# Optimization experiments

Measured on AMD Instinct MI355X. Metric: run time of the kernel, lower is better.

## Reference

```python
import jax, jax.numpy as jnp
import numpy as np

B, N_FED, INPUT_DIM, LATENT_DIM = 8192, 16384, 1024, 512


def setup_inputs() -> dict:
    key = jax.random.key(0)
    k1, k2, k3 = jax.random.split(key, 3)
    enc = jax.random.normal(k1, (B, LATENT_DIM), dtype=jnp.float32)
    X_fed = jax.random.normal(k2, (N_FED, INPUT_DIM), dtype=jnp.float32)
    # torch.rand -> uniform [0, 1)
    domain_diff = jax.random.uniform(k3, (INPUT_DIM, LATENT_DIM), dtype=jnp.float32)
    return {"enc": enc, "X_fed": X_fed, "domain_diff": domain_diff}


def reference(enc, X_fed, domain_diff):
    # K = V = X_fed @ domain_diff  (computed once; torch source computes it twice)
    kv = X_fed @ domain_diff                      # (N_fed, latent)
    scores = jnp.einsum('bd,nd->bn', enc, kv) / enc.shape[1]  # scale by latent_dim
    attn = jax.nn.softmax(scores, axis=1)         # softmax over N_fed axis
    z = attn @ kv                                 # (B, latent)
    return z
```

## Files before the change

kernel.cpp:

```cpp
#include <hip/hip_runtime.h>
#include <hip/hip_bf16.h>
#include <stdint.h>

#define ENC_B 8192
#define NFED  16384
#define INDIM 1024
#define LAT   512
#define SCALE (1.0f/512.0f)

typedef __attribute__((ext_vector_type(4))) float f32x4;
typedef __attribute__((ext_vector_type(8))) short short8;
typedef __attribute__((ext_vector_type(4))) short short4_t;

static __device__ __forceinline__ short f2bf(float x){
  union { float f; uint32_t u; } v; v.f = x;
  uint32_t r = v.u + 0x7FFFu + ((v.u >> 16) & 1u);
  return (short)(r >> 16);
}

static __device__ __forceinline__ void gload16(const void* g, void* l){
  __builtin_amdgcn_global_load_lds(
      (const __attribute__((address_space(1))) void*)g,
      (__attribute__((address_space(3))) void*)l, 16, 0, 0);
}

__global__ void ddT_kernel(const float* __restrict__ dd, short* __restrict__ ddT){
  const int n = blockIdx.x;
  for (int k = threadIdx.x; k < INDIM; k += 256)
    ddT[(size_t)n*INDIM + k] = f2bf(dd[(size_t)k*LAT + n]);
}

__global__ __launch_bounds__(256) void encb_kernel(const float* __restrict__ enc,
                                                   short* __restrict__ encb){
  const int gid = blockIdx.x*256 + threadIdx.x;
  const size_t base = (size_t)gid * 8;
  float4 v0 = *(const float4*)(enc + base);
  float4 v1 = *(const float4*)(enc + base + 4);
  short8 s;
  s[0]=f2bf(v0.x*SCALE); s[1]=f2bf(v0.y*SCALE); s[2]=f2bf(v0.z*SCALE); s[3]=f2bf(v0.w*SCALE);
  s[4]=f2bf(v1.x*SCALE); s[5]=f2bf(v1.y*SCALE); s[6]=f2bf(v1.z*SCALE); s[7]=f2bf(v1.w*SCALE);
  *(short8*)(encb + base) = s;
}

__global__ __launch_bounds__(256, 2) void kv_gemm_kernel(const float* __restrict__ X,
                                                         const short* __restrict__ ddT,
                                                         short* __restrict__ kv){
  __shared__ __align__(16) short As[128*40];
  __shared__ __align__(16) short Bs[128*40];
  const int t = threadIdx.x;
  const int lane = t & 63, w = t >> 6;
  const int lr = lane & 15, lg = lane >> 4;
  const int m0 = (blockIdx.x >> 2) * 128;
  const int n0 = (blockIdx.x & 3) * 128;
  const int wm = (w >> 1) * 64, wn = (w & 1) * 64;
  f32x4 acc[4][4];
  #pragma unroll
  for (int i=0;i<4;++i)
    #pragma unroll
    for (int j=0;j<4;++j) acc[i][j] = (f32x4){0.f,0.f,0.f,0.f};

  for (int k0 = 0; k0 < INDIM; k0 += 32) {
    #pragma unroll
    for (int i = 0; i < 4; ++i) {
      int idx = t + i*256;
      int row = idx >> 3, c4 = (idx & 7)*4;
      float4 v = *(const float4*)(X + (size_t)(m0+row)*INDIM + k0 + c4);
      short4_t s; s[0]=f2bf(v.x); s[1]=f2bf(v.y); s[2]=f2bf(v.z); s[3]=f2bf(v.w);
      *(short4_t*)(As + row*40 + c4) = s;
    }
    #pragma unroll
    for (int i = 0; i < 2; ++i) {
      int idx = t + i*256;
      int row = idx >> 2, c8 = (idx & 3)*8;
      *(uint4*)(Bs + row*40 + c8) = *(const uint4*)(ddT + (size_t)(n0+row)*INDIM + k0 + c8);
    }
    __syncthreads();
    short8 a[4], b[4];
    #pragma unroll
    for (int i=0;i<4;++i) a[i] = *(short8*)(As + (wm + i*16 + lr)*40 + lg*8);
    #pragma unroll
    for (int i=0;i<4;++i) b[i] = *(short8*)(Bs + (wn + i*16 + lr)*40 + lg*8);
    #pragma unroll
    for (int i=0;i<4;++i)
      #pragma unroll
      for (int j=0;j<4;++j)
        acc[i][j] = __builtin_amdgcn_mfma_f32_16x16x32_bf16(a[i], b[j], acc[i][j], 0,0,0);
    __syncthreads();
  }
  #pragma unroll
  for (int i=0;i<4;++i)
    #pragma unroll
    for (int j=0;j<4;++j)
      #pragma unroll
      for (int r=0;r<4;++r)
        kv[(size_t)(m0 + wm + i*16 + lg*4 + r)*LAT + n0 + wn + j*16 + lr] = f2bf(acc[i][j][r]);
}

__global__ __launch_bounds__(256) void kvT_kernel(const short* __restrict__ kv,
                                                  short* __restrict__ kvT){
  __shared__ short tile[64][72];
  const int t = threadIdx.x;
  const int bn = blockIdx.x & (NFED/64 - 1);
  const int bd = blockIdx.x / (NFED/64);
  #pragma unroll
  for (int i=0;i<2;++i){
    int idx = t + i*256; int row = idx >> 3, cc = (idx & 7)*8;
    *(uint4*)&tile[row][cc] = *(const uint4*)(kv + (size_t)(bn*64+row)*LAT + bd*64 + cc);
  }
  __syncthreads();
  #pragma unroll
  for (int i=0;i<2;++i){
    int idx = t + i*256; int drow = idx >> 3, nn = (idx & 7)*8;
    short8 v;
    #pragma unroll
    for (int j=0;j<8;++j) v[j] = tile[nn+j][drow];
    *(short8*)(kvT + (size_t)(bd*64+drow)*NFED + bn*64 + nn) = v;
  }
}

__global__ __launch_bounds__(256, 4) void s_gemm_kernel(const short* __restrict__ encb,
                                                        const short* __restrict__ kv,
                                                        short* __restrict__ Pc,
                                                        float* __restrict__ lpart,
                                                        int cbase, int chunk){
  __shared__ __align__(16) short As[128*32];
  __shared__ __align__(16) short Bs[128*32];
  __shared__ float lsum[128][2];
  const int t = threadIdx.x;
  const int lane = t & 63, w = t >> 6;
  const int lr = lane & 15, lg = lane >> 4;
  const int m0 = blockIdx.y * 128;
  const int n0g = cbase + blockIdx.x * 128;
  const int wm = (w >> 1) * 64, wn = (w & 1) * 64;

  const int sr = lane >> 2, sc = (lane & 3) * 8;
  const char* Asrc0 = (const char*)(encb + (size_t)(m0 + w*16      + sr)*LAT + sc);
  const char* Asrc1 = (const char*)(encb + (size_t)(m0 + (4+w)*16  + sr)*LAT + sc);
  const char* Bsrc0 = (const char*)(kv   + (size_t)(n0g + w*16     + sr)*LAT + sc);
  const char* Bsrc1 = (const char*)(kv   + (size_t)(n0g + (4+w)*16 + sr)*LAT + sc);
  char* AsD0 = (char*)As + w*1024;  char* AsD1 = (char*)As + (4+w)*1024;
  char* BsD0 = (char*)Bs + w*1024;  char* BsD1 = (char*)Bs + (4+w)*1024;

  f32x4 acc[4][4];
  #pragma unroll
  for (int i=0;i<4;++i)
    #pragma unroll
    for (int j=0;j<4;++j) acc[i][j] = (f32x4){0.f,0.f,0.f,0.f};

  for (int k0 = 0; k0 < LAT; k0 += 32) {
    gload16(Asrc0, AsD0); gload16(Asrc1, AsD1);
    gload16(Bsrc0, BsD0); gload16(Bsrc1, BsD1);
    Asrc0 += 64; Asrc1 += 64; Bsrc0 += 64; Bsrc1 += 64;
    __syncthreads();
    short8 a[4], b[4];
    #pragma unroll
    for (int i=0;i<4;++i) a[i] = *(short8*)((char*)As + (wm + i*16 + lr)*64 + lg*16);
    #pragma unroll
    for (int i=0;i<4;++i) b[i] = *(short8*)((char*)Bs + (wn + i*16 + lr)*64 + lg*16);
    #pragma unroll
    for (int i=0;i<4;++i)
      #pragma unroll
      for (int j=0;j<4;++j)
        acc[i][j] = __builtin_amdgcn_mfma_f32_16x16x32_bf16(a[i], b[j], acc[i][j], 0,0,0);
    __syncthreads();
  }

  float psum[4][4];
  #pragma unroll
  for (int i=0;i<4;++i)
    #pragma unroll
    for (int r=0;r<4;++r) psum[i][r] = 0.f;

  const int collocal0 = blockIdx.x * 128 + wn;
  #pragma unroll
  for (int i=0;i<4;++i)
    #pragma unroll
    for (int j=0;j<4;++j)
      #pragma unroll
      for (int r=0;r<4;++r) {
        float p = __expf(acc[i][j][r]);
        psum[i][r] += p;
        Pc[(size_t)(m0 + wm + i*16 + lg*4 + r)*chunk + collocal0 + j*16 + lr] = f2bf(p);
      }
  #pragma unroll
  for (int i=0;i<4;++i)
    #pragma unroll
    for (int r=0;r<4;++r) {
      float v = psum[i][r];
      v += __shfl_xor(v, 1, 16); v += __shfl_xor(v, 2, 16);
      v += __shfl_xor(v, 4, 16); v += __shfl_xor(v, 8, 16);
      if (lr == 0) lsum[wm + i*16 + lg*4 + r][w & 1] = v;
    }
  __syncthreads();
  if (t < 128) {
    int jsl = (cbase >> 7) + blockIdx.x;
    lpart[(size_t)jsl*ENC_B + m0 + t] = lsum[t][0] + lsum[t][1];
  }
}

__global__ __launch_bounds__(256, 4) void z_gemm_kernel(const short* __restrict__ kvT,
                                                        const short* __restrict__ Pc,
                                                        float* __restrict__ zpart,
                                                        int cbase, int chunk, int first){
  __shared__ __align__(16) short As[128*32];
  __shared__ __align__(16) short Bs[128*32];
  const int t = threadIdx.x;
  const int lane = t & 63, w = t >> 6;
  const int lr = lane & 15, lg = lane >> 4;
  const int n0 = blockIdx.x * 128;
  const int m0 = blockIdx.y * 128;
  const int s  = blockIdx.z;
  const int klocal0 = s * (chunk >> 2);
  const int wm = (w >> 1) * 64, wn = (w & 1) * 64;

  const int sr = lane >> 2, sc = (lane & 3) * 8;
  const char* Asrc0 = (const char*)(kvT + (size_t)(m0 + w*16      + sr)*NFED + cbase + klocal0 + sc);
  const char* Asrc1 = (const char*)(kvT + (size_t)(m0 + (4+w)*16  + sr)*NFED + cbase + klocal0 + sc);
  const char* Bsrc0 = (const char*)(Pc  + (size_t)(n0 + w*16      + sr)*chunk + klocal0 + sc);
  const char* Bsrc1 = (const char*)(Pc  + (size_t)(n0 + (4+w)*16  + sr)*chunk + klocal0 + sc);
  char* AsD0 = (char*)As + w*1024;  char* AsD1 = (char*)As + (4+w)*1024;
  char* BsD0 = (char*)Bs + w*1024;  char* BsD1 = (char*)Bs + (4+w)*1024;

  f32x4 acc[4][4];
  #pragma unroll
  for (int i=0;i<4;++i)
    #pragma unroll
    for (int j=0;j<4;++j) acc[i][j] = (f32x4){0.f,0.f,0.f,0.f};

  const int ksteps = chunk >> 7;
  for (int ks = 0; ks < ksteps; ++ks) {
    gload16(Asrc0, AsD0); gload16(Asrc1, AsD1);
    gload16(Bsrc0, BsD0); gload16(Bsrc1, BsD1);
    Asrc0 += 64; Asrc1 += 64; Bsrc0 += 64; Bsrc1 += 64;
    __syncthreads();
    short8 a[4], b[4];
    #pragma unroll
    for (int i=0;i<4;++i) a[i] = *(short8*)((char*)As + (wm + i*16 + lr)*64 + lg*16);
    #pragma unroll
    for (int i=0;i<4;++i) b[i] = *(short8*)((char*)Bs + (wn + i*16 + lr)*64 + lg*16);
    #pragma unroll
    for (int i=0;i<4;++i)
      #pragma unroll
      for (int j=0;j<4;++j)
        acc[i][j] = __builtin_amdgcn_mfma_f32_16x16x32_bf16(a[i], b[j], acc[i][j], 0,0,0);
    __syncthreads();
  }

  #pragma unroll
  for (int i=0;i<4;++i)
    #pragma unroll
    for (int j=0;j<4;++j)
      #pragma unroll
      for (int r=0;r<4;++r) {
        size_t idx = ((size_t)s*LAT + m0 + wm + i*16 + lg*4 + r)*ENC_B
                   + n0 + wn + j*16 + lr;
        if (first) zpart[idx] = acc[i][j][r];
        else       zpart[idx] += acc[i][j][r];
      }
}

__global__ __launch_bounds__(256) void lred_kernel(const float* __restrict__ lpart,
                                                   float* __restrict__ linv){
  const int row = blockIdx.x*256 + threadIdx.x;
  float sum = 0.f;
  for (int j = 0; j < NFED/128; ++j)
    sum += lpart[(size_t)j*ENC_B + row];
  linv[row] = 1.0f / sum;
}

__global__ __launch_bounds__(256) void zcomb_kernel(const float* __restrict__ zpart,
                                                    const float* __restrict__ linv,
                                                    float* __restrict__ out){
  __shared__ float tile[64][65];
  const int t = threadIdx.x;
  const int bx = blockIdx.x;
  const int by = blockIdx.y;
  const size_t sstr = (size_t)LAT*ENC_B;
  #pragma unroll
  for (int i=0;i<4;++i){
    int idx = t + i*256;
    int dr = idx >> 4, rc = (idx & 15)*4;
    const float* p0 = zpart + (size_t)(by*64+dr)*ENC_B + bx*64 + rc;
    float4 a = *(const float4*)p0;
    float4 b = *(const float4*)(p0 + sstr);
    float4 c = *(const float4*)(p0 + 2*sstr);
    float4 d = *(const float4*)(p0 + 3*sstr);
    tile[dr][rc+0] = (a.x+b.x)+(c.x+d.x); tile[dr][rc+1] = (a.y+b.y)+(c.y+d.y);
    tile[dr][rc+2] = (a.z+b.z)+(c.z+d.z); tile[dr][rc+3] = (a.w+b.w)+(c.w+d.w);
  }
  __syncthreads();
  #pragma unroll
  for (int i=0;i<4;++i){
    int idx = t + i*256;
    int rr = idx >> 4, dc = (idx & 15)*4;
    float li = linv[bx*64 + rr];
    float4 o;
    o.x = tile[dc+0][rr]*li; o.y = tile[dc+1][rr]*li;
    o.z = tile[dc+2][rr]*li; o.w = tile[dc+3][rr]*li;
    *(float4*)(out + (size_t)(bx*64+rr)*LAT + by*64 + dc) = o;
  }
}

extern "C" void kernel_launch(void* const* d_in, const int* in_sizes, int n_in,
                              void* d_out, int out_size, void* d_ws, size_t ws_size,
                              hipStream_t stream) {
  const float* enc = (const float*)d_in[0];
  const float* X   = (const float*)d_in[1];
  const float* dd  = (const float*)d_in[2];
  float* out = (float*)d_out;

  short* kvb   = (short*)d_ws;
  short* kvT   = (short*)((char*)d_ws + 16777216);
  short* encb  = (short*)((char*)d_ws + 33554432);
  float* lpart = (float*)((char*)d_ws + 41943040);
  short* ddT   = (short*)((char*)d_ws + 41943040);
  float* linv  = (float*)((char*)d_ws + 46137344);
  float* zpart = (float*)((char*)d_ws + 50331648);
  short* Pc    = (short*)((char*)d_ws + 117440512);

  int chunk;
  if      (ws_size >= (size_t)117440512 + (size_t)4096*ENC_B*2) chunk = 4096;
  else if (ws_size >= (size_t)117440512 + (size_t)2048*ENC_B*2) chunk = 2048;
  else                                                          chunk = 1024;

  ddT_kernel<<<LAT, 256, 0, stream>>>(dd, ddT);
  kv_gemm_kernel<<<(NFED/128)*(LAT/128), 256, 0, stream>>>(X, ddT, kvb);
  kvT_kernel<<<(NFED/64)*(LAT/64), 256, 0, stream>>>(kvb, kvT);
  encb_kernel<<<ENC_B*LAT/(256*8), 256, 0, stream>>>(enc, encb);

  const int nc = NFED / chunk;
  for (int c = 0; c < nc; ++c) {
    s_gemm_kernel<<<dim3(chunk/128, ENC_B/128), 256, 0, stream>>>(
        encb, kvb, Pc, lpart, c*chunk, chunk);
    z_gemm_kernel<<<dim3(ENC_B/128, LAT/128, 4), 256, 0, stream>>>(
        kvT, Pc, zpart, c*chunk, chunk, (c == 0) ? 1 : 0);
  }
  lred_kernel<<<ENC_B/256, 256, 0, stream>>>(lpart, linv);
  zcomb_kernel<<<dim3(ENC_B/64, LAT/64), 256, 0, stream>>>(zpart, linv, out);
}
```

Baseline: 503.7 us.

## Retile z GEMM with swizzled LDS, bf16 partials, and 8 split-K slices

The z GEMM tile changes from 128x128 with k=32 to 64x128 with k=64 per step. LDS stores use an XOR swizzle to avoid bank conflicts, and each K split is 2-way across 8 rotating slices. Partial sums are stored as bf16 instead of fp32, which halves partial-buffer traffic, and the combine kernel sums 8 slices. The cost is that repeated bf16 read-modify-write accumulation loses precision, and slice indexing assumes the chunk count is a multiple of 4 (with the c<4 first flag).

```diff
diff --git a/kernel.cpp b/kernel.cpp
--- a/kernel.cpp
+++ b/kernel.cpp
@@ -16,6 +16,9 @@
   union { float f; uint32_t u; } v; v.f = x;
   uint32_t r = v.u + 0x7FFFu + ((v.u >> 16) & 1u);
   return (short)(r >> 16);
+}
+static __device__ __forceinline__ float bf2f(short s){
+  union { float f; uint32_t u; } v; v.u = ((uint32_t)(unsigned short)s) << 16; return v.f;
 }
 
 static __device__ __forceinline__ void gload16(const void* g, void* l){
@@ -200,62 +203,92 @@
 
 __global__ __launch_bounds__(256, 4) void z_gemm_kernel(const short* __restrict__ kvT,
                                                         const short* __restrict__ Pc,
-                                                        float* __restrict__ zpart,
-                                                        int cbase, int chunk, int first){
-  __shared__ __align__(16) short As[128*32];
-  __shared__ __align__(16) short Bs[128*32];
+                                                        short* __restrict__ zb,
+                                                        int cbase, int chunk,
+                                                        int sliceBase, int first){
+  __shared__ __align__(16) short As[64*64];
+  __shared__ __align__(16) short Bs[128*64];
   const int t = threadIdx.x;
   const int lane = t & 63, w = t >> 6;
   const int lr = lane & 15, lg = lane >> 4;
   const int n0 = blockIdx.x * 128;
-  const int m0 = blockIdx.y * 128;
+  const int m0 = blockIdx.y * 64;
   const int s  = blockIdx.z;
-  const int klocal0 = s * (chunk >> 2);
-  const int wm = (w >> 1) * 64, wn = (w & 1) * 64;
-
-  const int sr = lane >> 2, sc = (lane & 3) * 8;
-  const char* Asrc0 = (const char*)(kvT + (size_t)(m0 + w*16      + sr)*NFED + cbase + klocal0 + sc);
-  const char* Asrc1 = (const char*)(kvT + (size_t)(m0 + (4+w)*16  + sr)*NFED + cbase + klocal0 + sc);
-  const char* Bsrc0 = (const char*)(Pc  + (size_t)(n0 + w*16      + sr)*chunk + klocal0 + sc);
-  const char* Bsrc1 = (const char*)(Pc  + (size_t)(n0 + (4+w)*16  + sr)*chunk + klocal0 + sc);
-  char* AsD0 = (char*)As + w*1024;  char* AsD1 = (char*)As + (4+w)*1024;
-  char* BsD0 = (char*)Bs + w*1024;  char* BsD1 = (char*)Bs + (4+w)*1024;
-
-  f32x4 acc[4][4];
-  #pragma unroll
-  for (int i=0;i<4;++i)
+  const int sl = sliceBase + s;
+  const int klocal0 = s * (chunk >> 1);
+
+  const short* Asrc[2];
+  #pragma unroll
+  for (int i=0;i<2;++i){
+    int ca = i*256 + w*64 + lane;
+    int row = ca >> 3;
+    int kcs = (lane & 7) ^ (row & 7);
+    Asrc[i] = kvT + (size_t)(m0 + row)*NFED + cbase + klocal0 + kcs*8;
+  }
+  const short* Bsrc[4];
+  #pragma unroll
+  for (int i=0;i<4;++i){
+    int ca = i*256 + w*64 + lane;
+    int row = ca >> 3;
+    int kcs = (lane & 7) ^ (row & 7);
+    Bsrc[i] = Pc + (size_t)(n0 + row)*chunk + klocal0 + kcs*8;
+  }
+
+  f32x4 acc[2][4];
+  #pragma unroll
+  for (int i=0;i<2;++i)
     #pragma unroll
     for (int j=0;j<4;++j) acc[i][j] = (f32x4){0.f,0.f,0.f,0.f};
 
   const int ksteps = chunk >> 7;
   for (int ks = 0; ks < ksteps; ++ks) {
-    gload16(Asrc0, AsD0); gload16(Asrc1, AsD1);
-    gload16(Bsrc0, BsD0); gload16(Bsrc1, BsD1);
-    Asrc0 += 64; Asrc1 += 64; Bsrc0 += 64; Bsrc1 += 64;
-    __syncthreads();
-    short8 a[4], b[4];
-    #pragma unroll
-    for (int i=0;i<4;++i) a[i] = *(short8*)((char*)As + (wm + i*16 + lr)*64 + lg*16);
-    #pragma unroll
-    for (int i=0;i<4;++i) b[i] = *(short8*)((char*)Bs + (wn + i*16 + lr)*64 + lg*16);
-    #pragma unroll
-    for (int i=0;i<4;++i)
-      #pragma unroll
-      for (int j=0;j<4;++j)
-        acc[i][j] = __builtin_amdgcn_mfma_f32_16x16x32_bf16(a[i], b[j], acc[i][j], 0,0,0);
-    __syncthreads();
-  }
-
-  #pragma unroll
-  for (int i=0;i<4;++i)
-    #pragma unroll
-    for (int j=0;j<4;++j)
+    #pragma unroll
+    for (int i=0;i<2;++i){
+      gload16(Asrc[i], (char*)As + i*4096 + w*1024);
+      Asrc[i] += 64;
+    }
+    #pragma unroll
+    for (int i=0;i<4;++i){
+      gload16(Bsrc[i], (char*)Bs + i*4096 + w*1024);
+      Bsrc[i] += 64;
+    }
+    __syncthreads();
+
+    #pragma unroll
+    for (int kk=0;kk<2;++kk){
+      const uint32_t kbyte = kk*64 + lg*16;
+      short8 a[4], b[2];
+      #pragma unroll
+      for (int dj=0;dj<4;++dj){
+        int row = dj*16 + lr;
+        a[dj] = *(short8*)((char*)As + row*128 + (kbyte ^ ((uint32_t)(row & 7) << 4)));
+      }
+      #pragma unroll
+      for (int ri=0;ri<2;++ri){
+        int row = w*32 + ri*16 + lr;
+        b[ri] = *(short8*)((char*)Bs + row*128 + (kbyte ^ ((uint32_t)(row & 7) << 4)));
+      }
+      #pragma unroll
+      for (int ri=0;ri<2;++ri)
+        #pragma unroll
+        for (int dj=0;dj<4;++dj)
+          acc[ri][dj] = __builtin_amdgcn_mfma_f32_16x16x32_bf16(a[dj], b[ri], acc[ri][dj], 0,0,0);
+    }
+    __syncthreads();
+  }
+
+  #pragma unroll
+  for (int ri=0;ri<2;++ri)
+    #pragma unroll
+    for (int dj=0;dj<4;++dj)
       #pragma unroll
       for (int r=0;r<4;++r) {
-        size_t idx = ((size_t)s*LAT + m0 + wm + i*16 + lg*4 + r)*ENC_B
-                   + n0 + wn + j*16 + lr;
-        if (first) zpart[idx] = acc[i][j][r];
-        else       zpart[idx] += acc[i][j][r];
+        int d    = m0 + dj*16 + lg*4 + r;
+        int rowq = n0 + w*32 + ri*16 + lr;
+        size_t idx = ((size_t)sl*LAT + d)*ENC_B + rowq;
+        float v = acc[ri][dj][r];
+        if (!first) v += bf2f(zb[idx]);
+        zb[idx] = f2bf(v);
       }
 }
 
@@ -268,25 +301,24 @@
   linv[row] = 1.0f / sum;
 }
 
-__global__ __launch_bounds__(256) void zcomb_kernel(const float* __restrict__ zpart,
+__global__ __launch_bounds__(256) void zcomb_kernel(const short* __restrict__ zb,
                                                     const float* __restrict__ linv,
                                                     float* __restrict__ out){
   __shared__ float tile[64][65];
   const int t = threadIdx.x;
   const int bx = blockIdx.x;
   const int by = blockIdx.y;
-  const size_t sstr = (size_t)LAT*ENC_B;
   #pragma unroll
   for (int i=0;i<4;++i){
     int idx = t + i*256;
     int dr = idx >> 4, rc = (idx & 15)*4;
-    const float* p0 = zpart + (size_t)(by*64+dr)*ENC_B + bx*64 + rc;
-    float4 a = *(const float4*)p0;
-    float4 b = *(const float4*)(p0 + sstr);
-    float4 c = *(const float4*)(p0 + 2*sstr);
-    float4 d = *(const float4*)(p0 + 3*sstr);
-    tile[dr][rc+0] = (a.x+b.x)+(c.x+d.x); tile[dr][rc+1] = (a.y+b.y)+(c.y+d.y);
-    tile[dr][rc+2] = (a.z+b.z)+(c.z+d.z); tile[dr][rc+3] = (a.w+b.w)+(c.w+d.w);
+    float s0=0.f, s1=0.f, s2=0.f, s3=0.f;
+    #pragma unroll
+    for (int sl=0; sl<8; ++sl){
+      short4_t v = *(const short4_t*)(zb + ((size_t)sl*LAT + by*64 + dr)*ENC_B + bx*64 + rc);
+      s0 += bf2f(v[0]); s1 += bf2f(v[1]); s2 += bf2f(v[2]); s3 += bf2f(v[3]);
+    }
+    tile[dr][rc+0]=s0; tile[dr][rc+1]=s1; tile[dr][rc+2]=s2; tile[dr][rc+3]=s3;
   }
   __syncthreads();
   #pragma unroll
@@ -315,7 +347,7 @@
   float* lpart = (float*)((char*)d_ws + 41943040);
   short* ddT   = (short*)((char*)d_ws + 41943040);
   float* linv  = (float*)((char*)d_ws + 46137344);
-  float* zpart = (float*)((char*)d_ws + 50331648);
+  short* zb    = (short*)((char*)d_ws + 50331648);
   short* Pc    = (short*)((char*)d_ws + 117440512);
 
   int chunk;
@@ -332,9 +364,9 @@
   for (int c = 0; c < nc; ++c) {
     s_gemm_kernel<<<dim3(chunk/128, ENC_B/128), 256, 0, stream>>>(
         encb, kvb, Pc, lpart, c*chunk, chunk);
-    z_gemm_kernel<<<dim3(ENC_B/128, LAT/128, 4), 256, 0, stream>>>(
-        kvT, Pc, zpart, c*chunk, chunk, (c == 0) ? 1 : 0);
+    z_gemm_kernel<<<dim3(ENC_B/128, LAT/64, 2), 256, 0, stream>>>(
+        kvT, Pc, zb, c*chunk, chunk, (c & 3)*2, (c < 4) ? 1 : 0);
   }
   lred_kernel<<<ENC_B/256, 256, 0, stream>>>(lpart, linv);
-  zcomb_kernel<<<dim3(ENC_B/64, LAT/64), 256, 0, stream>>>(zpart, linv, out);
-}
+  zcomb_kernel<<<dim3(ENC_B/64, LAT/64), 256, 0, stream>>>(zb, linv, out);
+}
```

New measurement: 435.8 us. -13.5%, faster.
